# Kernel optimization log

Measured on AMD Instinct MI355X. Metric: run time of the kernel, lower is better.

Reference implementation:

```python
import jax, jax.numpy as jnp
import numpy as np

N_NEWS = 200000
N_COMPANIES = 10000
N_EDGES = 640000
HIDDEN = 256


def setup_inputs() -> dict:
    key = jax.random.key(0)
    ks = jax.random.split(key, 7)
    scale = 1.0 / np.sqrt(HIDDEN)  # keep tanh out of full saturation
    news_x = jax.random.normal(ks[0], (N_NEWS, HIDDEN), dtype=jnp.float32)
    company_x = jax.random.normal(ks[1], (N_COMPANIES, HIDDEN), dtype=jnp.float32)
    W_news = jax.random.normal(ks[2], (HIDDEN, HIDDEN), dtype=jnp.float32) * scale
    W_company = jax.random.normal(ks[3], (HIDDEN, HIDDEN), dtype=jnp.float32) * scale
    v = jax.random.normal(ks[4], (HIDDEN,), dtype=jnp.float32) * scale
    src = jax.random.randint(ks[5], (N_EDGES,), 0, N_NEWS, dtype=jnp.int64)
    dst = jax.random.randint(ks[6], (N_EDGES,), 0, N_COMPANIES, dtype=jnp.int64)
    return {
        "news_x": news_x,
        "company_x": company_x,
        "W_news": W_news,
        "W_company": W_company,
        "v": v,
        "src": src,
        "dst": dst,
        "num_companies": N_COMPANIES,
    }


def reference(news_x, company_x, W_news, W_company, v, src, dst, num_companies):
    # Gather per-edge endpoint features, project (nn.Linear applies x @ W.T).
    news_part = news_x[src] @ W_news.T          # [E, H]
    company_part = company_x[dst] @ W_company.T  # [E, H]
    scores = jnp.tanh(news_part + company_part) @ v  # [E]

    # Segment-wise (per-company) numerically stable softmax over incoming edges.
    smax = jax.ops.segment_max(scores, dst, num_segments=num_companies)  # [C]
    scores_exp = jnp.exp(scores - smax[dst])                             # [E]
    denom = jax.ops.segment_sum(scores_exp, dst, num_segments=num_companies)[dst]
    weights = scores_exp / jnp.clip(denom, 1e-9)                         # [E]

    # Weighted scatter-add of raw news features into company slots.
    out = jax.ops.segment_sum(news_x[src] * weights[:, None], dst,
                              num_segments=num_companies)               # [C, H]
    return out
```

## Files before the change

### kernel.cpp

```cpp
#include <hip/hip_runtime.h>
#include <hip/hip_bf16.h>
#include <cmath>
#include <cstdint>


#define H 256

typedef __attribute__((ext_vector_type(8))) short bfrag;
typedef __attribute__((ext_vector_type(4))) float ffrag;

__device__ __forceinline__ ushort f2bf(float f) {
  uint u = __float_as_uint(f);
  uint r = u + 0x7FFFu + ((u >> 16) & 1u);
  return (ushort)(r >> 16);
}
__device__ __forceinline__ float bf2f(ushort h) {
  return __uint_as_float((uint)h << 16);
}

__global__ void prep_kernel(const float* __restrict__ Wn, const float* __restrict__ Wc,
                            ushort* __restrict__ WnHi, ushort* __restrict__ WnLo,
                            ushort* __restrict__ WcHi, ushort* __restrict__ WcLo,
                            const int* __restrict__ dst, int* __restrict__ counts, int E) {
  const int b = blockIdx.x, tid = threadIdx.x;
  if (b < 256) {
    int i = b * 256 + tid;
    float w = Wn[i];
    ushort h = f2bf(w);
    WnHi[i] = h;
    WnLo[i] = f2bf(w - bf2f(h));
  } else if (b < 512) {
    int i = (b - 256) * 256 + tid;
    float w = Wc[i];
    ushort h = f2bf(w);
    WcHi[i] = h;
    WcLo[i] = f2bf(w - bf2f(h));
  } else {
    int e = (b - 512) * 256 + tid;
    if (e < E) atomicAdd(&counts[dst[e]], 1);
  }
}

__global__ void scan_kernel(const int* __restrict__ counts, int* __restrict__ offsets,
                            int* __restrict__ cursor, int C) {
  __shared__ int wsum[16];
  int tid = threadIdx.x;
  int lane = tid & 63, wid = tid >> 6;
  int base = 0;
  for (int start = 0; start < C; start += 1024) {
    int idx = start + tid;
    int val = (idx < C) ? counts[idx] : 0;
    int x = val;
#pragma unroll
    for (int off = 1; off < 64; off <<= 1) {
      int y = __shfl_up(x, off);
      if (lane >= off) x += y;
    }
    if (lane == 63) wsum[wid] = x;
    __syncthreads();
    int add = base;
    for (int w = 0; w < wid; ++w) add += wsum[w];
    if (idx < C) {
      int excl = add + x - val;
      offsets[idx] = excl;
      cursor[idx]  = excl;
    }
    int tot = 0;
#pragma unroll
    for (int w = 0; w < 16; ++w) tot += wsum[w];
    __syncthreads();
    base += tot;
  }
  if (tid == 0) offsets[C] = base;
}

__global__ void fill_kernel(const int* __restrict__ src, const int* __restrict__ dst,
                            int* __restrict__ cursor, int* __restrict__ srcs_sorted, int E) {
  int e = blockIdx.x * blockDim.x + threadIdx.x;
  if (e < E) {
    int d = dst[e];
    int pos = atomicAdd(&cursor[d], 1);
    srcs_sorted[pos] = src[e];
  }
}

__global__ __launch_bounds__(1024, 1) void gemm_persist(
    const float* __restrict__ Xc, const ushort* __restrict__ WcHi,
    const ushort* __restrict__ WcLo, ushort* __restrict__ cproj, int MC, int GC,
    const float* __restrict__ Xn, const ushort* __restrict__ WnHi,
    const ushort* __restrict__ WnLo, ushort* __restrict__ nproj,
    ushort* __restrict__ nxbf, int MN) {
  constexpr int PITCH = 264;
  __shared__ ushort Xs[2][64 * PITCH];
  const int tid = threadIdx.x;
  const int wv = tid >> 6, lane = tid & 63;
  const int q = lane >> 4, nidx = lane & 15;
  const int GN = gridDim.x - GC;

  const float* X; const ushort *Whi, *Wlo; ushort *proj, *xb; int M, nb, lb;
  if ((int)blockIdx.x < GC) {
    X = Xc; Whi = WcHi; Wlo = WcLo; proj = cproj; xb = nullptr; M = MC;
    nb = GC; lb = blockIdx.x;
  } else {
    X = Xn; Whi = WnHi; Wlo = WnLo; proj = nproj; xb = nxbf; M = MN;
    nb = GN; lb = blockIdx.x - GC;
  }
  const int nt = (M + 63) >> 6;
  const int qt = nt / nb, rt = nt % nb;
  const int first = lb * qt + (lb < rt ? lb : rt);
  const int cnt = qt + (lb < rt ? 1 : 0);
  if (cnt <= 0) return;

  bfrag bhi[8], blo[8];
#pragma unroll
  for (int ks = 0; ks < 8; ++ks) {
    const size_t off = (size_t)(wv * 16 + nidx) * H + ks * 32 + q * 8;
    bhi[ks] = *(const bfrag*)(Whi + off);
    blo[ks] = *(const bfrag*)(Wlo + off);
  }

  float4 xr[4];
  auto load4 = [&](int tile) {
#pragma unroll
    for (int j = 0; j < 4; ++j) {
      const int flat = j * 4096 + tid * 4;
      int gr = tile * 64 + (flat >> 8);
      if (gr >= M) gr = M - 1;
      xr[j] = *(const float4*)(X + (size_t)gr * H + (flat & 255));
    }
  };
  auto writebuf = [&](int p, int tile) {
#pragma unroll
    for (int j = 0; j < 4; ++j) {
      const int flat = j * 4096 + tid * 4;
      const int r = flat >> 8, k = flat & 255;
      ushort4 b4;
      b4.x = f2bf(xr[j].x); b4.y = f2bf(xr[j].y);
      b4.z = f2bf(xr[j].z); b4.w = f2bf(xr[j].w);
      *(ushort4*)&Xs[p][r * PITCH + k] = b4;
      if (xb) {
        const int gr = tile * 64 + r;
        *(ushort4*)(xb + (size_t)gr * H + k) = b4;
      }
    }
  };

  load4(first);
  writebuf(0, first);
  int p = 0;
  for (int t = 0; t < cnt; ++t) {
    __syncthreads();
    const int tile = first + t;
    const bool more = (t + 1 < cnt);
    if (more) load4(tile + 1);

    ffrag acc[4];
#pragma unroll
    for (int i = 0; i < 4; ++i) acc[i] = (ffrag)(0.f);
#pragma unroll
    for (int ks = 0; ks < 8; ++ks) {
      bfrag a[4];
#pragma unroll
      for (int i = 0; i < 4; ++i)
        a[i] = *(const bfrag*)&Xs[p][(16 * i + nidx) * PITCH + ks * 32 + q * 8];
#pragma unroll
      for (int i = 0; i < 4; ++i) {
        acc[i] = __builtin_amdgcn_mfma_f32_16x16x32_bf16(a[i], bhi[ks], acc[i], 0, 0, 0);
        acc[i] = __builtin_amdgcn_mfma_f32_16x16x32_bf16(a[i], blo[ks], acc[i], 0, 0, 0);
      }
    }

    const int row0 = tile * 64;
#pragma unroll
    for (int i = 0; i < 4; ++i)
#pragma unroll
      for (int r = 0; r < 4; ++r) {
        const int grow = row0 + 16 * i + q * 4 + r;
        if (grow < M)
          proj[(size_t)grow * H + wv * 16 + nidx] = f2bf(acc[i][r]);
      }

    if (more) writebuf(p ^ 1, tile + 1);
    p ^= 1;
  }
}

__device__ __forceinline__ float fast_tanh(float x) {
  float e = __builtin_amdgcn_exp2f(x * 2.8853900817779268f);
  float t = __builtin_amdgcn_rcpf(e + 1.f);
  return __builtin_fmaf(-2.f, t, 1.f);
}

__global__ __launch_bounds__(256) void edge_flash_kernel(
    const ushort* __restrict__ news_projbf, const ushort* __restrict__ company_projbf,
    const float* __restrict__ v, const int* __restrict__ offsets,
    const int* __restrict__ srcs, const ushort* __restrict__ news_xbf,
    float* __restrict__ out) {
  const int c = blockIdx.x;
  const int tid = threadIdx.x;
  const int sl = tid & 31;
  const int hw = tid >> 5;
  __shared__ float cp[H];
  __shared__ float mW[8], lW[8];
  __shared__ float OW[8][H];
  cp[tid] = bf2f(company_projbf[(size_t)c * H + tid]);
  __syncthreads();
  const float4 va = *(const float4*)(v + sl * 8);
  const float4 vb = *(const float4*)(v + sl * 8 + 4);
  const float4 ca = *(const float4*)&cp[sl * 8];
  const float4 cb = *(const float4*)&cp[sl * 8 + 4];
  const float vv[8] = {va.x, va.y, va.z, va.w, vb.x, vb.y, vb.z, vb.w};
  const float cq[8] = {ca.x, ca.y, ca.z, ca.w, cb.x, cb.y, cb.z, cb.w};
  const int beg = offsets[c], end = offsets[c + 1];

  float m = -INFINITY, l = 0.f;
  float O[8] = {0.f, 0.f, 0.f, 0.f, 0.f, 0.f, 0.f, 0.f};

  int i = beg + hw;
  if (i < end) {
    int s = srcs[i];
    bfrag pr = *(const bfrag*)(news_projbf + (size_t)s * H + sl * 8);
    bfrag xr = *(const bfrag*)(news_xbf + (size_t)s * H + sl * 8);
    for (;;) {
      const int inext = i + 8;
      const bool more = (inext < end);
      bfrag prn, xrn;
      if (more) {
        int sn = srcs[inext];
        prn = *(const bfrag*)(news_projbf + (size_t)sn * H + sl * 8);
        xrn = *(const bfrag*)(news_xbf + (size_t)sn * H + sl * 8);
      }
      float r = 0.f;
#pragma unroll
      for (int j = 0; j < 8; ++j)
        r += fast_tanh(bf2f((ushort)pr[j]) + cq[j]) * vv[j];
#pragma unroll
      for (int off = 16; off > 0; off >>= 1) r += __shfl_xor(r, off);
      const float mnew = fmaxf(m, r);
      const float alpha = __expf(m - mnew);
      const float pa = __expf(r - mnew);
      l = l * alpha + pa;
#pragma unroll
      for (int j = 0; j < 8; ++j)
        O[j] = O[j] * alpha + pa * bf2f((ushort)xr[j]);
      m = mnew;
      i = inext;
      if (!more) break;
      pr = prn; xr = xrn;
    }
  }

  if (sl == 0) { mW[hw] = m; lW[hw] = l; }
  *(float4*)&OW[hw][sl * 8]     = make_float4(O[0], O[1], O[2], O[3]);
  *(float4*)&OW[hw][sl * 8 + 4] = make_float4(O[4], O[5], O[6], O[7]);
  __syncthreads();
  float mstar = -INFINITY;
#pragma unroll
  for (int w = 0; w < 8; ++w) mstar = fmaxf(mstar, mW[w]);
  float denom = 0.f, val = 0.f;
#pragma unroll
  for (int w = 0; w < 8; ++w) {
    const float sc = (lW[w] > 0.f) ? __expf(mW[w] - mstar) : 0.f;
    denom += lW[w] * sc;
    val += OW[w][tid] * sc;
  }
  out[(size_t)c * H + tid] = val / fmaxf(denom, 1e-9f);
}

extern "C" void kernel_launch(void* const* d_in, const int* in_sizes, int n_in,
                              void* d_out, int out_size, void* d_ws, size_t ws_size,
                              hipStream_t stream) {
  const float* news_x    = (const float*)d_in[0];
  const float* company_x = (const float*)d_in[1];
  const float* W_news    = (const float*)d_in[2];
  const float* W_company = (const float*)d_in[3];
  const float* v         = (const float*)d_in[4];
  const int*   src       = (const int*)d_in[5];
  const int*   dst       = (const int*)d_in[6];
  const int N = in_sizes[0] / H;
  const int C = in_sizes[1] / H;
  const int E = in_sizes[5];
  float* out = (float*)d_out;

  char* p = (char*)d_ws;
  ushort* news_projbf    = (ushort*)p; p += (size_t)N * H * sizeof(ushort);
  ushort* news_xbf       = (ushort*)p; p += (size_t)N * H * sizeof(ushort);
  ushort* company_projbf = (ushort*)p; p += (size_t)C * H * sizeof(ushort);
  int*    srcs_sorted    = (int*)p;    p += (size_t)E * sizeof(int);
  ushort* Wn_hi          = (ushort*)p; p += (size_t)H * H * sizeof(ushort);
  ushort* Wn_lo          = (ushort*)p; p += (size_t)H * H * sizeof(ushort);
  ushort* Wc_hi          = (ushort*)p; p += (size_t)H * H * sizeof(ushort);
  ushort* Wc_lo          = (ushort*)p; p += (size_t)H * H * sizeof(ushort);
  int*    counts         = (int*)p;    p += (size_t)C * sizeof(int);
  int*    offsets        = (int*)p;    p += (size_t)(C + 1) * sizeof(int);
  int*    cursor         = (int*)p;    p += (size_t)C * sizeof(int);

  hipMemsetAsync(counts, 0, (size_t)C * sizeof(int), stream);
  prep_kernel<<<512 + (E + 255) / 256, 256, 0, stream>>>(
      W_news, W_company, Wn_hi, Wn_lo, Wc_hi, Wc_lo, dst, counts, E);
  scan_kernel<<<1, 1024, 0, stream>>>(counts, offsets, cursor, C);
  fill_kernel<<<(E + 255) / 256, 256, 0, stream>>>(src, dst, cursor, srcs_sorted, E);

  const int GC = 24, GN = 488;
  gemm_persist<<<GC + GN, 1024, 0, stream>>>(
      company_x, Wc_hi, Wc_lo, company_projbf, C, GC,
      news_x, Wn_hi, Wn_lo, news_projbf, news_xbf, N);

  edge_flash_kernel<<<C, 256, 0, stream>>>(news_projbf, company_projbf, v, offsets,
                                           srcs_sorted, news_xbf, out);
}
```

Before: 535.3 us.

## Fuse CSR fill and weight bf16 split into persistent GEMM kernel

Removes the separate fill kernel and the weight hi/lo bf16 conversion from the prep kernel. Each persistent GEMM block now scatters its slice of edges into the sorted-source array before starting, and converts its fp32 weight fragments to hi/lo bf16 in registers. The goal is to cut launches and the intermediate weight buffers. In exchange every block redoes the weight conversion and front-loads atomic scatter work ahead of its GEMM tiles.

```diff
diff --git a/kernel.cpp b/kernel.cpp
--- a/kernel.cpp
+++ b/kernel.cpp
@@ -18,27 +18,9 @@
   return __uint_as_float((uint)h << 16);
 }
 
-__global__ void prep_kernel(const float* __restrict__ Wn, const float* __restrict__ Wc,
-                            ushort* __restrict__ WnHi, ushort* __restrict__ WnLo,
-                            ushort* __restrict__ WcHi, ushort* __restrict__ WcLo,
-                            const int* __restrict__ dst, int* __restrict__ counts, int E) {
-  const int b = blockIdx.x, tid = threadIdx.x;
-  if (b < 256) {
-    int i = b * 256 + tid;
-    float w = Wn[i];
-    ushort h = f2bf(w);
-    WnHi[i] = h;
-    WnLo[i] = f2bf(w - bf2f(h));
-  } else if (b < 512) {
-    int i = (b - 256) * 256 + tid;
-    float w = Wc[i];
-    ushort h = f2bf(w);
-    WcHi[i] = h;
-    WcLo[i] = f2bf(w - bf2f(h));
-  } else {
-    int e = (b - 512) * 256 + tid;
-    if (e < E) atomicAdd(&counts[dst[e]], 1);
-  }
+__global__ void hist_kernel(const int* __restrict__ dst, int* __restrict__ counts, int E) {
+  int e = blockIdx.x * blockDim.x + threadIdx.x;
+  if (e < E) atomicAdd(&counts[dst[e]], 1);
 }
 
 __global__ void scan_kernel(const int* __restrict__ counts, int* __restrict__ offsets,
@@ -74,22 +56,13 @@
   if (tid == 0) offsets[C] = base;
 }
 
-__global__ void fill_kernel(const int* __restrict__ src, const int* __restrict__ dst,
-                            int* __restrict__ cursor, int* __restrict__ srcs_sorted, int E) {
-  int e = blockIdx.x * blockDim.x + threadIdx.x;
-  if (e < E) {
-    int d = dst[e];
-    int pos = atomicAdd(&cursor[d], 1);
-    srcs_sorted[pos] = src[e];
-  }
-}
-
 __global__ __launch_bounds__(1024, 1) void gemm_persist(
-    const float* __restrict__ Xc, const ushort* __restrict__ WcHi,
-    const ushort* __restrict__ WcLo, ushort* __restrict__ cproj, int MC, int GC,
-    const float* __restrict__ Xn, const ushort* __restrict__ WnHi,
-    const ushort* __restrict__ WnLo, ushort* __restrict__ nproj,
-    ushort* __restrict__ nxbf, int MN) {
+    const float* __restrict__ Xc, const float* __restrict__ Wc,
+    ushort* __restrict__ cproj, int MC, int GC,
+    const float* __restrict__ Xn, const float* __restrict__ Wn,
+    ushort* __restrict__ nproj, ushort* __restrict__ nxbf, int MN,
+    const int* __restrict__ esrc, const int* __restrict__ edst,
+    int* __restrict__ cursor, int* __restrict__ srcs_sorted, int E) {
   constexpr int PITCH = 264;
   __shared__ ushort Xs[2][64 * PITCH];
   const int tid = threadIdx.x;
@@ -97,12 +70,23 @@
   const int q = lane >> 4, nidx = lane & 15;
   const int GN = gridDim.x - GC;
 
-  const float* X; const ushort *Whi, *Wlo; ushort *proj, *xb; int M, nb, lb;
+  {
+    const int B = gridDim.x;
+    const int e0 = (int)(((long long)blockIdx.x * E) / B);
+    const int e1 = (int)(((long long)(blockIdx.x + 1) * E) / B);
+    for (int e = e0 + tid; e < e1; e += 1024) {
+      const int d = edst[e];
+      const int pos = atomicAdd(&cursor[d], 1);
+      srcs_sorted[pos] = esrc[e];
+    }
+  }
+
+  const float* X; const float* W; ushort *proj, *xb; int M, nb, lb;
   if ((int)blockIdx.x < GC) {
-    X = Xc; Whi = WcHi; Wlo = WcLo; proj = cproj; xb = nullptr; M = MC;
+    X = Xc; W = Wc; proj = cproj; xb = nullptr; M = MC;
     nb = GC; lb = blockIdx.x;
   } else {
-    X = Xn; Whi = WnHi; Wlo = WnLo; proj = nproj; xb = nxbf; M = MN;
+    X = Xn; W = Wn; proj = nproj; xb = nxbf; M = MN;
     nb = GN; lb = blockIdx.x - GC;
   }
   const int nt = (M + 63) >> 6;
@@ -112,11 +96,20 @@
   if (cnt <= 0) return;
 
   bfrag bhi[8], blo[8];
-#pragma unroll
-  for (int ks = 0; ks < 8; ++ks) {
-    const size_t off = (size_t)(wv * 16 + nidx) * H + ks * 32 + q * 8;
-    bhi[ks] = *(const bfrag*)(Whi + off);
-    blo[ks] = *(const bfrag*)(Wlo + off);
+  {
+    const float* Wp = W + (size_t)(wv * 16 + nidx) * H + q * 8;
+#pragma unroll
+    for (int ks = 0; ks < 8; ++ks) {
+      const float4 w0 = *(const float4*)(Wp + ks * 32);
+      const float4 w1 = *(const float4*)(Wp + ks * 32 + 4);
+      const float wf[8] = {w0.x, w0.y, w0.z, w0.w, w1.x, w1.y, w1.z, w1.w};
+#pragma unroll
+      for (int j = 0; j < 8; ++j) {
+        const ushort h = f2bf(wf[j]);
+        bhi[ks][j] = (short)h;
+        blo[ks][j] = (short)f2bf(wf[j] - bf2f(h));
+      }
+    }
   }
 
   float4 xr[4];
@@ -287,24 +280,19 @@
   ushort* news_xbf       = (ushort*)p; p += (size_t)N * H * sizeof(ushort);
   ushort* company_projbf = (ushort*)p; p += (size_t)C * H * sizeof(ushort);
   int*    srcs_sorted    = (int*)p;    p += (size_t)E * sizeof(int);
-  ushort* Wn_hi          = (ushort*)p; p += (size_t)H * H * sizeof(ushort);
-  ushort* Wn_lo          = (ushort*)p; p += (size_t)H * H * sizeof(ushort);
-  ushort* Wc_hi          = (ushort*)p; p += (size_t)H * H * sizeof(ushort);
-  ushort* Wc_lo          = (ushort*)p; p += (size_t)H * H * sizeof(ushort);
   int*    counts         = (int*)p;    p += (size_t)C * sizeof(int);
   int*    offsets        = (int*)p;    p += (size_t)(C + 1) * sizeof(int);
   int*    cursor         = (int*)p;    p += (size_t)C * sizeof(int);
 
   hipMemsetAsync(counts, 0, (size_t)C * sizeof(int), stream);
-  prep_kernel<<<512 + (E + 255) / 256, 256, 0, stream>>>(
-      W_news, W_company, Wn_hi, Wn_lo, Wc_hi, Wc_lo, dst, counts, E);
+  hist_kernel<<<(E + 255) / 256, 256, 0, stream>>>(dst, counts, E);
   scan_kernel<<<1, 1024, 0, stream>>>(counts, offsets, cursor, C);
-  fill_kernel<<<(E + 255) / 256, 256, 0, stream>>>(src, dst, cursor, srcs_sorted, E);
 
   const int GC = 24, GN = 488;
   gemm_persist<<<GC + GN, 1024, 0, stream>>>(
-      company_x, Wc_hi, Wc_lo, company_projbf, C, GC,
-      news_x, Wn_hi, Wn_lo, news_projbf, news_xbf, N);
+      company_x, W_company, company_projbf, C, GC,
+      news_x, W_news, news_projbf, news_xbf, N,
+      src, dst, cursor, srcs_sorted, E);
 
   edge_flash_kernel<<<C, 256, 0, stream>>>(news_projbf, company_projbf, v, offsets,
                                            srcs_sorted, news_xbf, out);
```

Measured after the change: 558.4 us. 1.04x slower.
